# Kernel optimization log

Measured on AMD Instinct MI355X. Metric: run time of the kernel, lower is better.

Reference implementation:

```python
import jax, jax.numpy as jnp
import numpy as np

NT, NS, NH = 1096, 2048, 16

def setup_inputs() -> dict:
    key = jax.random.key(0)
    ks = jax.random.split(key, 6)
    # precipitation (non-negative) and temperature (can be +/-)
    P = jax.random.uniform(ks[0], (NT, NS), dtype=jnp.float32) * 10.0
    T = jax.random.normal(ks[1], (NT, NS), dtype=jnp.float32) * 10.0
    w_i = jax.random.uniform(ks[2], (NH,), minval=-1.0, maxval=1.0, dtype=jnp.float32)
    w_o = jax.random.uniform(ks[3], (NH,), minval=-1.0, maxval=1.0, dtype=jnp.float32)
    w_l = jax.random.uniform(ks[4], (NH,), minval=-1.0, maxval=1.0, dtype=jnp.float32)  # LinearBucket.w
    w_s = jax.random.uniform(ks[5], (NH,), minval=-1.0, maxval=2.0, dtype=jnp.float32)  # SnowBucket.w
    return dict(P=P, T=T, w_i=w_i, w_o=w_o, w_l=w_l, w_s=w_s)


def reference(P, T, w_i, w_o, w_l, w_s):
    # Time-invariant gate factors (Dropout is identity in eval mode)
    melt_coef = jnp.exp(w_s) + 1.0          # [nh]
    gi = jax.nn.sigmoid(w_i)                # [nh] input gate
    gl = jax.nn.sigmoid(w_l)                # [nh] linear-bucket release fraction
    a = jax.nn.softmax(w_o)                 # [nh] output mixing weights

    ns = P.shape[1]
    nh = w_i.shape[0]
    s0 = jnp.zeros((ns, nh), P.dtype)
    h0 = jnp.zeros((ns, nh), P.dtype)

    def step(carry, pt):
        s, h = carry
        Pk, Tk = pt                          # [ns]
        # SnowBucket (nm=0: melt m = min(potential melt, snow store))
        sm = jax.nn.relu(Tk)[:, None] * melt_coef      # [ns, nh]
        m = jnp.minimum(sm, s)
        sn = s - m + jnp.where(Tk < 0, Pk, 0.0)[:, None]
        x = jnp.where(Tk > 0, Pk, 0.0)[:, None] + m
        # input gate + LinearBucket
        xin = x * gi
        q = (xin + h) * gl
        hn = h - q + xin
        Qk = jnp.sum(q * a, axis=1)                    # [ns]
        return (sn, hn), (Qk, hn, sn)

    _, (Q, H, S) = jax.lax.scan(step, (s0, h0), (P, T))
    return Q, H, S
```

## Files before the change

kernel.cpp:

```cpp
#include <hip/hip_runtime.h>


constexpr int NT = 1096;
constexpr int NS = 2048;
constexpr int NH = 16;
constexpr int NSH = NS * NH;
constexpr int NC = 8;
constexpr int L  = NT / NC;
static_assert(NC * L == NT, "NT must divide into NC chunks exactly");
constexpr int PF = 8;

__device__ __forceinline__ float sigm(float x) { return 1.0f / (1.0f + expf(-x)); }

__global__ __launch_bounds__(256) void k_scanA(
    const float* __restrict__ P, const float* __restrict__ T,
    const float* __restrict__ wsb,
    float* __restrict__ outA, float* __restrict__ outB)
{
    const int gid  = blockIdx.x * 256 + (int)threadIdx.x;
    const int hh   = gid & (NH - 1);
    const int site = (gid >> 4) & (NS - 1);
    const int c    = gid >> 15;

    const float mcv = expf(wsb[hh]) + 1.0f;
    const int t0 = c * L;

    float pf[PF], tf[PF];
    #pragma unroll
    for (int k = 0; k < PF; ++k) {
        pf[k] = P[(t0 + k) * NS + site];
        tf[k] = T[(t0 + k) * NS + site];
    }

    float A = 0.0f, B = -1e38f;
    auto step = [&](float Pk, float Tk) {
        const float tpos = fmaxf(Tk, 0.0f);
        const float pn   = (Tk < 0.0f) ? Pk : 0.0f;
        const float at   = pn - tpos * mcv;
        A += at;
        B = fmaxf(B + at, pn);
    };

    int base = 0;
    for (; base + PF <= L; base += PF) {
        #pragma unroll
        for (int k = 0; k < PF; ++k) {
            const float Pk = pf[k], Tk = tf[k];
            int tn = t0 + base + k + PF;
            tn = min(tn, NT - 1);
            pf[k] = P[tn * NS + site];
            tf[k] = T[tn * NS + site];
            step(Pk, Tk);
        }
    }
    #pragma unroll
    for (int k = 0; k < PF; ++k) {
        if (base + k < L) step(pf[k], tf[k]);
    }

    outA[gid] = A;
    outB[gid] = B;
}

__global__ __launch_bounds__(256) void k_resolveS(
    const float* __restrict__ A, const float* __restrict__ B,
    float* __restrict__ S0)
{
    const int idx = blockIdx.x * 256 + (int)threadIdx.x;
    float a[NC], b[NC];
    #pragma unroll
    for (int c = 0; c < NC; ++c) {
        a[c] = A[c * NSH + idx];
        b[c] = B[c * NSH + idx];
    }
    float s = 0.0f;
    #pragma unroll
    for (int c = 0; c < NC; ++c) {
        S0[c * NSH + idx] = s;
        s = fmaxf(s + a[c], b[c]);
    }
}

__global__ __launch_bounds__(256) void k_scanH(
    const float* __restrict__ P, const float* __restrict__ T,
    const float* __restrict__ wi, const float* __restrict__ wl,
    const float* __restrict__ wsb,
    const float* __restrict__ S0, float* __restrict__ HP)
{
    const int gid  = blockIdx.x * 256 + (int)threadIdx.x;
    const int hh   = gid & (NH - 1);
    const int site = (gid >> 4) & (NS - 1);
    const int c    = gid >> 15;

    const float mcv = expf(wsb[hh]) + 1.0f;
    const float giv = sigm(wi[hh]);
    const float clv = 1.0f - sigm(wl[hh]);

    float s  = S0[gid];
    float hp = 0.0f;

    const int t0 = c * L;
    float pf[PF], tf[PF];
    #pragma unroll
    for (int k = 0; k < PF; ++k) {
        pf[k] = P[(t0 + k) * NS + site];
        tf[k] = T[(t0 + k) * NS + site];
    }

    auto step = [&](float Pk, float Tk) {
        const float tpos = fmaxf(Tk, 0.0f);
        const float pnn  = (Tk < 0.0f) ? Pk : 0.0f;
        const float ppp  = (Tk > 0.0f) ? Pk : 0.0f;
        const float smv  = tpos * mcv;
        const float m    = fminf(smv, s);
        s = s - m + pnn;
        const float xin  = (ppp + m) * giv;
        hp = clv * (hp + xin);
    };

    int base = 0;
    for (; base + PF <= L; base += PF) {
        #pragma unroll
        for (int k = 0; k < PF; ++k) {
            const float Pk = pf[k], Tk = tf[k];
            int tn = t0 + base + k + PF;
            tn = min(tn, NT - 1);
            pf[k] = P[tn * NS + site];
            tf[k] = T[tn * NS + site];
            step(Pk, Tk);
        }
    }
    #pragma unroll
    for (int k = 0; k < PF; ++k) {
        if (base + k < L) step(pf[k], tf[k]);
    }

    HP[gid] = hp;
}

__global__ __launch_bounds__(256) void k_resolveH(
    const float* __restrict__ wl, const float* __restrict__ HP,
    float* __restrict__ H0)
{
    const int idx = blockIdx.x * 256 + (int)threadIdx.x;
    const float cl  = 1.0f - sigm(wl[idx & (NH - 1)]);
    const float clL = powf(cl, (float)L);
    float hp[NC];
    #pragma unroll
    for (int c = 0; c < NC; ++c) hp[c] = HP[c * NSH + idx];
    float h = 0.0f;
    #pragma unroll
    for (int c = 0; c < NC; ++c) {
        H0[c * NSH + idx] = h;
        h = clL * h + hp[c];
    }
}

__global__ __launch_bounds__(256) void k_final(
    const float* __restrict__ P, const float* __restrict__ T,
    const float* __restrict__ wi, const float* __restrict__ wo,
    const float* __restrict__ wl, const float* __restrict__ wsb,
    const float* __restrict__ S0, const float* __restrict__ H0,
    float* __restrict__ Q, float* __restrict__ H, float* __restrict__ S)
{
    const int gid  = blockIdx.x * 256 + (int)threadIdx.x;
    const int hh   = gid & (NH - 1);
    const int site = (gid >> 4) & (NS - 1);
    const int c    = gid >> 15;
    const int lidx = gid & (NSH - 1);

    const float mcv = expf(wsb[hh]) + 1.0f;
    const float giv = sigm(wi[hh]);
    const float glv = sigm(wl[hh]);
    float mx = -1e30f;
    #pragma unroll
    for (int j = 0; j < NH; ++j) mx = fmaxf(mx, wo[j]);
    float den = 0.0f;
    #pragma unroll
    for (int j = 0; j < NH; ++j) den += expf(wo[j] - mx);
    const float aw = expf(wo[hh] - mx) / den;

    float s = S0[gid];
    float h = H0[gid];

    const int t0 = c * L;
    float pf[PF], tf[PF];
    #pragma unroll
    for (int k = 0; k < PF; ++k) {
        pf[k] = P[(t0 + k) * NS + site];
        tf[k] = T[(t0 + k) * NS + site];
    }

    auto step = [&](float Pk, float Tk, int ta) {
        const float tpos = fmaxf(Tk, 0.0f);
        const float pnn  = (Tk < 0.0f) ? Pk : 0.0f;
        const float ppp  = (Tk > 0.0f) ? Pk : 0.0f;
        const float smv  = tpos * mcv;
        const float m    = fminf(smv, s);
        s = s - m + pnn;
        const float xin  = (ppp + m) * giv;
        const float q    = (xin + h) * glv;
        h = h - q + xin;
        float qa = q * aw;
        qa += __shfl_xor(qa, 1, 16);
        qa += __shfl_xor(qa, 2, 16);
        qa += __shfl_xor(qa, 4, 16);
        qa += __shfl_xor(qa, 8, 16);
        const int ofs = ta * NSH + lidx;
        S[ofs] = s;
        H[ofs] = h;
        if (hh == 0) Q[ta * NS + site] = qa;
    };

    int base = 0;
    for (; base + PF <= L; base += PF) {
        #pragma unroll
        for (int k = 0; k < PF; ++k) {
            const float Pk = pf[k], Tk = tf[k];
            int tn = t0 + base + k + PF;
            tn = min(tn, NT - 1);
            pf[k] = P[tn * NS + site];
            tf[k] = T[tn * NS + site];
            step(Pk, Tk, t0 + base + k);
        }
    }
    #pragma unroll
    for (int k = 0; k < PF; ++k) {
        if (base + k < L) step(pf[k], tf[k], t0 + base + k);
    }
}

__global__ __launch_bounds__(64) void waternet_seq(
    const float* __restrict__ P, const float* __restrict__ T,
    const float* __restrict__ w_i, const float* __restrict__ w_o,
    const float* __restrict__ w_l, const float* __restrict__ w_s,
    float* __restrict__ Q, float* __restrict__ H, float* __restrict__ S)
{
    const int gid = blockIdx.x * 64 + (int)threadIdx.x;
    const int hh = gid & (NH - 1);
    const int site = gid >> 4;
    const float melt_coef = expf(w_s[hh]) + 1.0f;
    const float gi = sigm(w_i[hh]);
    const float gl = sigm(w_l[hh]);
    float mx = -1e30f;
    for (int j = 0; j < NH; ++j) mx = fmaxf(mx, w_o[j]);
    float denom = 0.0f;
    for (int j = 0; j < NH; ++j) denom += expf(w_o[j] - mx);
    const float a = expf(w_o[hh] - mx) / denom;
    float s = 0.0f, h = 0.0f;
    for (int t = 0; t < NT; ++t) {
        const float Pk = P[t * NS + site];
        const float Tk = T[t * NS + site];
        const float sm = fmaxf(Tk, 0.0f) * melt_coef;
        const float m = fminf(sm, s);
        s = s - m + ((Tk < 0.0f) ? Pk : 0.0f);
        const float xin = (((Tk > 0.0f) ? Pk : 0.0f) + m) * gi;
        const float q = (xin + h) * gl;
        h = h - q + xin;
        const int ofs = t * NSH + gid;
        S[ofs] = s; H[ofs] = h;
        float qa = q * a;
        qa += __shfl_xor(qa, 1, 16);
        qa += __shfl_xor(qa, 2, 16);
        qa += __shfl_xor(qa, 4, 16);
        qa += __shfl_xor(qa, 8, 16);
        if (hh == 0) Q[t * NS + site] = qa;
    }
}

extern "C" void kernel_launch(void* const* d_in, const int* in_sizes, int n_in,
                              void* d_out, int out_size, void* d_ws, size_t ws_size,
                              hipStream_t stream) {
    const float* P   = (const float*)d_in[0];
    const float* T   = (const float*)d_in[1];
    const float* w_i = (const float*)d_in[2];
    const float* w_o = (const float*)d_in[3];
    const float* w_l = (const float*)d_in[4];
    const float* w_s = (const float*)d_in[5];

    float* Q = (float*)d_out;
    float* H = Q + (size_t)NT * NS;
    float* S = H + (size_t)NT * NS * NH;

    const size_t need = 3ull * NC * NSH * sizeof(float);
    if (ws_size < need) {
        waternet_seq<<<(NS * NH) / 64, 64, 0, stream>>>(P, T, w_i, w_o, w_l, w_s, Q, H, S);
        return;
    }

    float* buf0 = (float*)d_ws;
    float* buf1 = buf0 + (size_t)NC * NSH;
    float* buf2 = buf1 + (size_t)NC * NSH;

    const int nblk = (NC * NSH) / 256;
    const int rblk = NSH / 256;

    k_scanA   <<<nblk, 256, 0, stream>>>(P, T, w_s, buf0, buf1);
    k_resolveS<<<rblk, 256, 0, stream>>>(buf0, buf1, buf2);
    k_scanH   <<<nblk, 256, 0, stream>>>(P, T, w_i, w_l, w_s, buf2, buf0);
    k_resolveH<<<rblk, 256, 0, stream>>>(w_l, buf0, buf1);
    k_final   <<<nblk, 256, 0, stream>>>(P, T, w_i, w_o, w_l, w_s, buf2, buf1,
                                         Q, H, S);
}
```

Measured before the change: 359.5 us.

## Fuse chunked scan pipeline into one per-site kernel with LDS-staged inputs

Replaces the five-kernel chunked scan (two scans, two resolves, final pass through global workspace) with a single kernel where each block handles one site, 32 time chunks by 16 heads. P/T for the site are staged once into shared memory and the chunk carries are resolved in LDS between barriers. S is written during the H-partial pass, so the final pass writes only H and Q. This removes launch overhead, workspace round trips and repeated global reads of P/T. In exchange the store pattern becomes one site's 16 heads per chunk, giving 64-byte scattered writes, and the tiny serial resolve loops run on only 16 threads.

```diff
diff --git a/kernel.cpp b/kernel.cpp
--- a/kernel.cpp
+++ b/kernel.cpp
@@ -1,270 +1,131 @@
 #include <hip/hip_runtime.h>
 
 
-constexpr int NT = 1096;
-constexpr int NS = 2048;
-constexpr int NH = 16;
+constexpr int NT  = 1096;
+constexpr int NS  = 2048;
+constexpr int NH  = 16;
 constexpr int NSH = NS * NH;
-constexpr int NC = 8;
-constexpr int L  = NT / NC;
-static_assert(NC * L == NT, "NT must divide into NC chunks exactly");
-constexpr int PF = 8;
+constexpr int NC  = 32;
+constexpr int LCH = (NT + NC - 1) / NC;
+constexpr int BT  = NC * NH;
 
 __device__ __forceinline__ float sigm(float x) { return 1.0f / (1.0f + expf(-x)); }
 
-__global__ __launch_bounds__(256) void k_scanA(
-    const float* __restrict__ P, const float* __restrict__ T,
-    const float* __restrict__ wsb,
-    float* __restrict__ outA, float* __restrict__ outB)
-{
-    const int gid  = blockIdx.x * 256 + (int)threadIdx.x;
-    const int hh   = gid & (NH - 1);
-    const int site = (gid >> 4) & (NS - 1);
-    const int c    = gid >> 15;
-
-    const float mcv = expf(wsb[hh]) + 1.0f;
-    const int t0 = c * L;
-
-    float pf[PF], tf[PF];
-    #pragma unroll
-    for (int k = 0; k < PF; ++k) {
-        pf[k] = P[(t0 + k) * NS + site];
-        tf[k] = T[(t0 + k) * NS + site];
-    }
-
-    float A = 0.0f, B = -1e38f;
-    auto step = [&](float Pk, float Tk) {
-        const float tpos = fmaxf(Tk, 0.0f);
-        const float pn   = (Tk < 0.0f) ? Pk : 0.0f;
-        const float at   = pn - tpos * mcv;
-        A += at;
-        B = fmaxf(B + at, pn);
-    };
-
-    int base = 0;
-    for (; base + PF <= L; base += PF) {
-        #pragma unroll
-        for (int k = 0; k < PF; ++k) {
-            const float Pk = pf[k], Tk = tf[k];
-            int tn = t0 + base + k + PF;
-            tn = min(tn, NT - 1);
-            pf[k] = P[tn * NS + site];
-            tf[k] = T[tn * NS + site];
-            step(Pk, Tk);
-        }
-    }
-    #pragma unroll
-    for (int k = 0; k < PF; ++k) {
-        if (base + k < L) step(pf[k], tf[k]);
-    }
-
-    outA[gid] = A;
-    outB[gid] = B;
-}
-
-__global__ __launch_bounds__(256) void k_resolveS(
-    const float* __restrict__ A, const float* __restrict__ B,
-    float* __restrict__ S0)
-{
-    const int idx = blockIdx.x * 256 + (int)threadIdx.x;
-    float a[NC], b[NC];
-    #pragma unroll
-    for (int c = 0; c < NC; ++c) {
-        a[c] = A[c * NSH + idx];
-        b[c] = B[c * NSH + idx];
-    }
-    float s = 0.0f;
-    #pragma unroll
-    for (int c = 0; c < NC; ++c) {
-        S0[c * NSH + idx] = s;
-        s = fmaxf(s + a[c], b[c]);
-    }
-}
-
-__global__ __launch_bounds__(256) void k_scanH(
-    const float* __restrict__ P, const float* __restrict__ T,
-    const float* __restrict__ wi, const float* __restrict__ wl,
-    const float* __restrict__ wsb,
-    const float* __restrict__ S0, float* __restrict__ HP)
-{
-    const int gid  = blockIdx.x * 256 + (int)threadIdx.x;
-    const int hh   = gid & (NH - 1);
-    const int site = (gid >> 4) & (NS - 1);
-    const int c    = gid >> 15;
-
-    const float mcv = expf(wsb[hh]) + 1.0f;
-    const float giv = sigm(wi[hh]);
-    const float clv = 1.0f - sigm(wl[hh]);
-
-    float s  = S0[gid];
-    float hp = 0.0f;
-
-    const int t0 = c * L;
-    float pf[PF], tf[PF];
-    #pragma unroll
-    for (int k = 0; k < PF; ++k) {
-        pf[k] = P[(t0 + k) * NS + site];
-        tf[k] = T[(t0 + k) * NS + site];
-    }
-
-    auto step = [&](float Pk, float Tk) {
-        const float tpos = fmaxf(Tk, 0.0f);
-        const float pnn  = (Tk < 0.0f) ? Pk : 0.0f;
-        const float ppp  = (Tk > 0.0f) ? Pk : 0.0f;
-        const float smv  = tpos * mcv;
-        const float m    = fminf(smv, s);
-        s = s - m + pnn;
-        const float xin  = (ppp + m) * giv;
-        hp = clv * (hp + xin);
-    };
-
-    int base = 0;
-    for (; base + PF <= L; base += PF) {
-        #pragma unroll
-        for (int k = 0; k < PF; ++k) {
-            const float Pk = pf[k], Tk = tf[k];
-            int tn = t0 + base + k + PF;
-            tn = min(tn, NT - 1);
-            pf[k] = P[tn * NS + site];
-            tf[k] = T[tn * NS + site];
-            step(Pk, Tk);
-        }
-    }
-    #pragma unroll
-    for (int k = 0; k < PF; ++k) {
-        if (base + k < L) step(pf[k], tf[k]);
-    }
-
-    HP[gid] = hp;
-}
-
-__global__ __launch_bounds__(256) void k_resolveH(
-    const float* __restrict__ wl, const float* __restrict__ HP,
-    float* __restrict__ H0)
-{
-    const int idx = blockIdx.x * 256 + (int)threadIdx.x;
-    const float cl  = 1.0f - sigm(wl[idx & (NH - 1)]);
-    const float clL = powf(cl, (float)L);
-    float hp[NC];
-    #pragma unroll
-    for (int c = 0; c < NC; ++c) hp[c] = HP[c * NSH + idx];
-    float h = 0.0f;
-    #pragma unroll
-    for (int c = 0; c < NC; ++c) {
-        H0[c * NSH + idx] = h;
-        h = clL * h + hp[c];
-    }
-}
-
-__global__ __launch_bounds__(256) void k_final(
-    const float* __restrict__ P, const float* __restrict__ T,
-    const float* __restrict__ wi, const float* __restrict__ wo,
-    const float* __restrict__ wl, const float* __restrict__ wsb,
-    const float* __restrict__ S0, const float* __restrict__ H0,
-    float* __restrict__ Q, float* __restrict__ H, float* __restrict__ S)
-{
-    const int gid  = blockIdx.x * 256 + (int)threadIdx.x;
-    const int hh   = gid & (NH - 1);
-    const int site = (gid >> 4) & (NS - 1);
-    const int c    = gid >> 15;
-    const int lidx = gid & (NSH - 1);
-
-    const float mcv = expf(wsb[hh]) + 1.0f;
-    const float giv = sigm(wi[hh]);
-    const float glv = sigm(wl[hh]);
-    float mx = -1e30f;
-    #pragma unroll
-    for (int j = 0; j < NH; ++j) mx = fmaxf(mx, wo[j]);
-    float den = 0.0f;
-    #pragma unroll
-    for (int j = 0; j < NH; ++j) den += expf(wo[j] - mx);
-    const float aw = expf(wo[hh] - mx) / den;
-
-    float s = S0[gid];
-    float h = H0[gid];
-
-    const int t0 = c * L;
-    float pf[PF], tf[PF];
-    #pragma unroll
-    for (int k = 0; k < PF; ++k) {
-        pf[k] = P[(t0 + k) * NS + site];
-        tf[k] = T[(t0 + k) * NS + site];
-    }
-
-    auto step = [&](float Pk, float Tk, int ta) {
-        const float tpos = fmaxf(Tk, 0.0f);
-        const float pnn  = (Tk < 0.0f) ? Pk : 0.0f;
-        const float ppp  = (Tk > 0.0f) ? Pk : 0.0f;
-        const float smv  = tpos * mcv;
-        const float m    = fminf(smv, s);
-        s = s - m + pnn;
-        const float xin  = (ppp + m) * giv;
-        const float q    = (xin + h) * glv;
-        h = h - q + xin;
-        float qa = q * aw;
-        qa += __shfl_xor(qa, 1, 16);
-        qa += __shfl_xor(qa, 2, 16);
-        qa += __shfl_xor(qa, 4, 16);
-        qa += __shfl_xor(qa, 8, 16);
-        const int ofs = ta * NSH + lidx;
-        S[ofs] = s;
-        H[ofs] = h;
-        if (hh == 0) Q[ta * NS + site] = qa;
-    };
-
-    int base = 0;
-    for (; base + PF <= L; base += PF) {
-        #pragma unroll
-        for (int k = 0; k < PF; ++k) {
-            const float Pk = pf[k], Tk = tf[k];
-            int tn = t0 + base + k + PF;
-            tn = min(tn, NT - 1);
-            pf[k] = P[tn * NS + site];
-            tf[k] = T[tn * NS + site];
-            step(Pk, Tk, t0 + base + k);
-        }
-    }
-    #pragma unroll
-    for (int k = 0; k < PF; ++k) {
-        if (base + k < L) step(pf[k], tf[k], t0 + base + k);
-    }
-}
-
-__global__ __launch_bounds__(64) void waternet_seq(
+__global__ __launch_bounds__(BT) void waternet_fused(
     const float* __restrict__ P, const float* __restrict__ T,
     const float* __restrict__ w_i, const float* __restrict__ w_o,
     const float* __restrict__ w_l, const float* __restrict__ w_s,
     float* __restrict__ Q, float* __restrict__ H, float* __restrict__ S)
 {
-    const int gid = blockIdx.x * 64 + (int)threadIdx.x;
-    const int hh = gid & (NH - 1);
-    const int site = gid >> 4;
-    const float melt_coef = expf(w_s[hh]) + 1.0f;
+    __shared__ float2 PT[NT];
+    __shared__ float bufA[BT];
+    __shared__ float bufB[BT];
+    __shared__ float bufC[BT];
+
+    const int tid  = (int)threadIdx.x;
+    const int hh   = tid & (NH - 1);
+    const int c    = tid >> 4;
+    const int site = (int)blockIdx.x;
+
+    for (int t = tid; t < NT; t += BT) {
+        const float p  = P[(size_t)t * NS + site];
+        const float tt = T[(size_t)t * NS + site];
+        PT[t] = make_float2(p, tt);
+    }
+
+    const float mc = expf(w_s[hh]) + 1.0f;
     const float gi = sigm(w_i[hh]);
     const float gl = sigm(w_l[hh]);
+    const float cl = 1.0f - gl;
+
+    const int t0  = c * LCH;
+    const int len = min(NT - t0, LCH);
+
+    __syncthreads();
+
+    float A = 0.0f, B = -1e38f;
+    for (int i = 0; i < len; ++i) {
+        const float2 pt = PT[t0 + i];
+        const float tpos = fmaxf(pt.y, 0.0f);
+        const float pnn  = (pt.y < 0.0f) ? pt.x : 0.0f;
+        const float at   = pnn - tpos * mc;
+        A += at;
+        B = fmaxf(B + at, pnn);
+    }
+    bufA[tid] = A;
+    bufB[tid] = B;
+    __syncthreads();
+
+    if (tid < NH) {
+        float s = 0.0f;
+        for (int k = 0; k < NC; ++k) {
+            bufC[k * NH + tid] = s;
+            s = fmaxf(s + bufA[k * NH + tid], bufB[k * NH + tid]);
+        }
+    }
+    __syncthreads();
+
+    float s = bufC[tid];
+    float hp = 0.0f;
+    {
+        float* Sp = S + (size_t)t0 * NSH + (size_t)site * NH + hh;
+        for (int i = 0; i < len; ++i) {
+            const float2 pt = PT[t0 + i];
+            const float tpos = fmaxf(pt.y, 0.0f);
+            const float pnn  = (pt.y < 0.0f) ? pt.x : 0.0f;
+            const float ppp  = (pt.y > 0.0f) ? pt.x : 0.0f;
+            const float m    = fminf(tpos * mc, s);
+            s = s - m + pnn;
+            Sp[(size_t)i * NSH] = s;
+            const float xin = (ppp + m) * gi;
+            hp = cl * (hp + xin);
+        }
+    }
+    bufA[tid] = hp;
+    __syncthreads();
+
+    if (tid < NH) {
+        const float clr = 1.0f - sigm(w_l[tid]);
+        float h = 0.0f;
+        for (int k = 0; k < NC; ++k) {
+            bufB[k * NH + tid] = h;
+            const int lk = min(NT - k * LCH, LCH);
+            h = powf(clr, (float)lk) * h + bufA[k * NH + tid];
+        }
+    }
+    __syncthreads();
+
     float mx = -1e30f;
+    #pragma unroll
     for (int j = 0; j < NH; ++j) mx = fmaxf(mx, w_o[j]);
-    float denom = 0.0f;
-    for (int j = 0; j < NH; ++j) denom += expf(w_o[j] - mx);
-    const float a = expf(w_o[hh] - mx) / denom;
-    float s = 0.0f, h = 0.0f;
-    for (int t = 0; t < NT; ++t) {
-        const float Pk = P[t * NS + site];
-        const float Tk = T[t * NS + site];
-        const float sm = fmaxf(Tk, 0.0f) * melt_coef;
-        const float m = fminf(sm, s);
-        s = s - m + ((Tk < 0.0f) ? Pk : 0.0f);
-        const float xin = (((Tk > 0.0f) ? Pk : 0.0f) + m) * gi;
-        const float q = (xin + h) * gl;
-        h = h - q + xin;
-        const int ofs = t * NSH + gid;
-        S[ofs] = s; H[ofs] = h;
-        float qa = q * a;
-        qa += __shfl_xor(qa, 1, 16);
-        qa += __shfl_xor(qa, 2, 16);
-        qa += __shfl_xor(qa, 4, 16);
-        qa += __shfl_xor(qa, 8, 16);
-        if (hh == 0) Q[t * NS + site] = qa;
+    float den = 0.0f;
+    #pragma unroll
+    for (int j = 0; j < NH; ++j) den += expf(w_o[j] - mx);
+    const float aw = expf(w_o[hh] - mx) / den;
+
+    s = bufC[tid];
+    float h = bufB[tid];
+    {
+        float* Hp = H + (size_t)t0 * NSH + (size_t)site * NH + hh;
+        float* Qp = Q + (size_t)t0 * NS + site;
+        for (int i = 0; i < len; ++i) {
+            const float2 pt = PT[t0 + i];
+            const float tpos = fmaxf(pt.y, 0.0f);
+            const float pnn  = (pt.y < 0.0f) ? pt.x : 0.0f;
+            const float ppp  = (pt.y > 0.0f) ? pt.x : 0.0f;
+            const float m    = fminf(tpos * mc, s);
+            s = s - m + pnn;
+            const float xin = (ppp + m) * gi;
+            const float q   = (xin + h) * gl;
+            h = cl * (h + xin);
+            Hp[(size_t)i * NSH] = h;
+            float qa = q * aw;
+            qa += __shfl_xor(qa, 1, 16);
+            qa += __shfl_xor(qa, 2, 16);
+            qa += __shfl_xor(qa, 4, 16);
+            qa += __shfl_xor(qa, 8, 16);
+            if (hh == 0) Qp[(size_t)i * NS] = qa;
+        }
     }
 }
 
@@ -282,23 +143,5 @@
     float* H = Q + (size_t)NT * NS;
     float* S = H + (size_t)NT * NS * NH;
 
-    const size_t need = 3ull * NC * NSH * sizeof(float);
-    if (ws_size < need) {
-        waternet_seq<<<(NS * NH) / 64, 64, 0, stream>>>(P, T, w_i, w_o, w_l, w_s, Q, H, S);
-        return;
-    }
-
-    float* buf0 = (float*)d_ws;
-    float* buf1 = buf0 + (size_t)NC * NSH;
-    float* buf2 = buf1 + (size_t)NC * NSH;
-
-    const int nblk = (NC * NSH) / 256;
-    const int rblk = NSH / 256;
-
-    k_scanA   <<<nblk, 256, 0, stream>>>(P, T, w_s, buf0, buf1);
-    k_resolveS<<<rblk, 256, 0, stream>>>(buf0, buf1, buf2);
-    k_scanH   <<<nblk, 256, 0, stream>>>(P, T, w_i, w_l, w_s, buf2, buf0);
-    k_resolveH<<<rblk, 256, 0, stream>>>(w_l, buf0, buf1);
-    k_final   <<<nblk, 256, 0, stream>>>(P, T, w_i, w_o, w_l, w_s, buf2, buf1,
-                                         Q, H, S);
+    waternet_fused<<<NS, BT, 0, stream>>>(P, T, w_i, w_o, w_l, w_s, Q, H, S);
 }
```

New measurement: 410.3 us. +14.1%, slower.
